# Performance work log

Hardware: AMD Instinct MI355X
Metric: run time of the kernel (lower is better)

Reference implementation:

```python
import jax, jax.numpy as jnp
import numpy as np
import math

B, S_IN, S_OUT, D_IN, D_OUT, G = 8, 1024, 1024, 96, 96, 8
LN_EPS = 1e-5


def setup_inputs() -> dict:
    key = jax.random.key(0)
    k_x, k_m, k_p, k_l = jax.random.split(key, 4)
    x = jax.random.normal(k_x, (B, S_IN, D_IN), dtype=jnp.float32)
    M = jax.random.uniform(k_m, (D_OUT, D_IN), minval=-0.5, maxval=0.5, dtype=jnp.float32)
    P = jax.random.uniform(k_p, (D_OUT, D_OUT, G), minval=-0.1, maxval=0.1, dtype=jnp.float32)
    Linker = jax.random.uniform(k_l, (S_IN, S_OUT), minval=-0.1, maxval=0.1, dtype=jnp.float32)
    gamma = jnp.ones((D_OUT,), dtype=jnp.float32)
    beta = jnp.zeros((D_OUT,), dtype=jnp.float32)
    return {"x": x, "M": M, "P": P, "Linker": Linker, "gamma": gamma, "beta": beta}


def _layer_norm(z, gamma, beta):
    mu = jnp.mean(z, axis=-1, keepdims=True)
    var = jnp.mean(jnp.square(z - mu), axis=-1, keepdims=True)
    return (z - mu) * jax.lax.rsqrt(var + LN_EPS) * gamma + beta


def reference(x, M, P, Linker, gamma, beta):
    # Z = x @ M^T, then LayerNorm over feature dim
    Z0 = jnp.einsum('bsj,ij->bsi', x, M)           # (B, S_in, D_out)
    Z = _layer_norm(Z0, gamma, beta)
    # periods[i,j,g] = i*(D_out*G) + j*G + g + 2
    periods = (jnp.arange(D_OUT * D_OUT * G, dtype=jnp.float32)
               .reshape(D_OUT, D_OUT, G) + 2.0)
    k = jnp.arange(S_IN, dtype=jnp.float32)
    # phi[s,i,j,g] = cos(2*pi*s / periods[i,j,g])
    phi = jnp.cos((2.0 * math.pi) * k[:, None, None, None] / periods[None])
    # fuse basis reduction: W[s,i,j] = sum_g P[i,j,g] * phi[s,i,j,g]
    W = jnp.einsum('sijg,ijg->sij', phi, P)        # (S_in, D_out, D_out)
    # T[b,s,i] = sum_j Z[b,s,j] * W[s,i,j]
    T = jnp.einsum('bsj,sij->bsi', Z, W)           # (B, S_in, D_out)
    # sequence transform via Linker
    U = jnp.einsum('bsi,st->bti', T, Linker)       # (B, S_out, D_out)
    # shared residual: x @ M^T (pre-LN) through the same Linker
    residual = jnp.einsum('bsi,st->bti', Z0, Linker)
    return U + residual
```

## Files before the change

### kernel.cpp

```cpp
#include <hip/hip_runtime.h>
#include <cstdint>
#include <cstddef>

#define NPAIR 9216
#define BSTRIDE 98304

typedef __attribute__((ext_vector_type(8))) short short8;
typedef __attribute__((ext_vector_type(4))) float f32x4;

__device__ __forceinline__ uint16_t f2bf(float x) {
    uint32_t u = __float_as_uint(x);
    return (uint16_t)((u + 0x7FFF + ((u >> 16) & 1)) >> 16);
}
__device__ __forceinline__ float bf2f(uint16_t b) {
    return __uint_as_float(((uint32_t)b) << 16);
}

union SmemK1 {
    float M[96][97];
    struct { float zb[16][100]; float ps[16][6][2]; float stats[16][2]; } ln;
    struct { float T[64][65]; } kl;
};

__global__ __launch_bounds__(96) void k1_mega(
    const float* __restrict__ x, const float* __restrict__ M,
    const float* __restrict__ P, const float* __restrict__ L,
    const float* __restrict__ gamma, const float* __restrict__ beta,
    float* __restrict__ Z0, float* __restrict__ Z,
    uint16_t* __restrict__ Lt, uint16_t* __restrict__ Wt)
{
    __shared__ SmemK1 sm;
    const int t  = threadIdx.x;
    const int bx = blockIdx.x;

    if (bx < 512) {
        const int R0 = bx * 16;
        for (int k = 0; k < 24; ++k) {
            int mm = t + 96 * k;
            int i = mm / 24, j0 = (mm % 24) * 4;
            float4 v = *(const float4*)(M + i * 96 + j0);
            sm.M[i][j0]   = v.x; sm.M[i][j0+1] = v.y;
            sm.M[i][j0+2] = v.z; sm.M[i][j0+3] = v.w;
        }
        __syncthreads();
        float mreg[96];
        #pragma unroll
        for (int j = 0; j < 96; ++j) mreg[j] = sm.M[t][j];
        __syncthreads();

        for (int r = 0; r < 16; ++r) {
            const float* xr = x + (size_t)(R0 + r) * 96;
            float a0 = 0.f, a1 = 0.f, a2 = 0.f, a3 = 0.f;
            #pragma unroll
            for (int j = 0; j < 96; j += 4) {
                a0 = fmaf(xr[j+0], mreg[j+0], a0);
                a1 = fmaf(xr[j+1], mreg[j+1], a1);
                a2 = fmaf(xr[j+2], mreg[j+2], a2);
                a3 = fmaf(xr[j+3], mreg[j+3], a3);
            }
            float z = (a0 + a1) + (a2 + a3);
            sm.ln.zb[r][t] = z;
            Z0[(size_t)(R0 + r) * 96 + t] = z;
        }
        __syncthreads();
        {
            const int row = t / 6, seg = t % 6;
            const float4* zp = (const float4*)&sm.ln.zb[row][seg * 16];
            float s1 = 0.f, s2 = 0.f;
            #pragma unroll
            for (int k = 0; k < 4; ++k) {
                float4 v = zp[k];
                s1 += v.x + v.y + v.z + v.w;
                s2 += v.x*v.x + v.y*v.y + v.z*v.z + v.w*v.w;
            }
            sm.ln.ps[row][seg][0] = s1;
            sm.ln.ps[row][seg][1] = s2;
        }
        __syncthreads();
        if (t < 16) {
            float s1 = 0.f, s2 = 0.f;
            #pragma unroll
            for (int k = 0; k < 6; ++k) {
                s1 += sm.ln.ps[t][k][0];
                s2 += sm.ln.ps[t][k][1];
            }
            float mu  = s1 * (1.f / 96.f);
            float var = s2 * (1.f / 96.f) - mu * mu;
            sm.ln.stats[t][0] = mu;
            sm.ln.stats[t][1] = rsqrtf(var + 1e-5f);
        }
        __syncthreads();
        {
            float gm = gamma[t], bt = beta[t];
            for (int r = 0; r < 16; ++r) {
                float mu = sm.ln.stats[r][0], rs = sm.ln.stats[r][1];
                Z[(size_t)(R0 + r) * 96 + t] =
                    (sm.ln.zb[r][t] - mu) * rs * gm + bt;
            }
        }
        return;
    }

    if (bx < 768) {
        const int bx2 = bx - 512;
        const int s0 = (bx2 & 15) * 64, t0 = (bx2 >> 4) * 64;
        if (t < 64) {
            for (int r = 0; r < 64; ++r)
                sm.kl.T[r][t] = L[(size_t)(s0 + r) * 1024 + t0 + t];
        }
        __syncthreads();
        if (t < 64) {
            uint16_t* orow = Lt + (size_t)(t0 + t) * 1024 + s0;
            #pragma unroll
            for (int c4 = 0; c4 < 16; ++c4) {
                uint32_t u01 = (uint32_t)f2bf(sm.kl.T[c4*4+0][t]) |
                               ((uint32_t)f2bf(sm.kl.T[c4*4+1][t]) << 16);
                uint32_t u23 = (uint32_t)f2bf(sm.kl.T[c4*4+2][t]) |
                               ((uint32_t)f2bf(sm.kl.T[c4*4+3][t]) << 16);
                uint2 o; o.x = u01; o.y = u23;
                *(uint2*)(orow + c4 * 4) = o;
            }
        }
        return;
    }

    {
        const int idx = bx - 768;
        const int pb  = idx % 96;
        const int sc  = idx / 96;
        const int p   = pb * 96 + t;
        const int i   = p % 96, j = p / 96;
        const int s0  = sc * 64;
        const int base = (i * 96 + j) * 8;

        float Pv[8], c[8], cp[8], tc1[8];
        {
            float4 a = *(const float4*)(P + base);
            float4 b = *(const float4*)(P + base + 4);
            Pv[0]=a.x; Pv[1]=a.y; Pv[2]=a.z; Pv[3]=a.w;
            Pv[4]=b.x; Pv[5]=b.y; Pv[6]=b.z; Pv[7]=b.w;
        }
        #pragma unroll
        for (int g = 0; g < 8; ++g) {
            float inv = 1.0f / (float)(base + g + 2);
            float c1  = cospif(2.0f * inv);
            tc1[g] = c1 + c1;
            c[g]  = cospif(2.0f * (float)s0 * inv);
            cp[g] = cospif(2.0f * (float)(s0 - 1) * inv);
        }
        uint16_t* op = Wt + (size_t)s0 * NPAIR + p;
        for (int ss = 0; ss < 64; ++ss) {
            float w = 0.f;
            #pragma unroll
            for (int g = 0; g < 8; ++g) w = fmaf(Pv[g], c[g], w);
            *op = f2bf(w);
            op += NPAIR;
            #pragma unroll
            for (int g = 0; g < 8; ++g) {
                float cn = fmaf(tc1[g], c[g], -cp[g]);
                cp[g] = c[g]; c[g] = cn;
            }
        }
    }
}

__global__ __launch_bounds__(96) void kt_apply(
    const float* __restrict__ Z, const float* __restrict__ Z0,
    const uint16_t* __restrict__ Wt, uint16_t* __restrict__ Vt)
{
    const int i = threadIdx.x;
    const int s = blockIdx.x;
    float acc[8] = {0.f,0.f,0.f,0.f,0.f,0.f,0.f,0.f};
    const uint16_t* wrow = Wt + (size_t)s * NPAIR + i;
    const float* zs = Z + (size_t)s * 96;
    #pragma unroll 8
    for (int j = 0; j < 96; ++j) {
        float w = bf2f(wrow[j * 96]);
        #pragma unroll
        for (int bb = 0; bb < 8; ++bb)
            acc[bb] = fmaf(zs[(size_t)bb * BSTRIDE + j], w, acc[bb]);
    }
    #pragma unroll
    for (int bb = 0; bb < 8; ++bb) {
        size_t o = (size_t)bb * BSTRIDE + (size_t)s * 96 + i;
        Vt[((size_t)bb * 96 + i) * 1024 + s] = f2bf(acc[bb] + Z0[o]);
    }
}

__global__ __launch_bounds__(128) void k3_mfma(
    const uint16_t* __restrict__ Lt, const uint16_t* __restrict__ Vt,
    float* __restrict__ out)
{
    const int lane = threadIdx.x & 63;
    const int wv   = threadIdx.x >> 6;
    const int m    = lane & 15;
    const int quad = lane >> 4;
    const int t0   = blockIdx.x * 32 + wv * 16;
    const int b    = blockIdx.y;

    const uint16_t* Lp = Lt + (size_t)(t0 + m) * 1024 + quad * 8;
    const uint16_t* Vp = Vt + ((size_t)b * 96 + m) * 1024 + quad * 8;

    f32x4 acc[6];
    #pragma unroll
    for (int ii = 0; ii < 6; ++ii) acc[ii] = (f32x4){0.f, 0.f, 0.f, 0.f};

    short8 a = *(const short8*)Lp;
    short8 bv[6];
    #pragma unroll
    for (int ii = 0; ii < 6; ++ii)
        bv[ii] = *(const short8*)(Vp + (size_t)ii * 16 * 1024);

    for (int kc = 0; kc < 31; ++kc) {
        short8 an = *(const short8*)(Lp + (kc + 1) * 32);
        short8 bn[6];
        #pragma unroll
        for (int ii = 0; ii < 6; ++ii)
            bn[ii] = *(const short8*)(Vp + (size_t)ii * 16 * 1024 + (kc + 1) * 32);
        #pragma unroll
        for (int ii = 0; ii < 6; ++ii)
            acc[ii] = __builtin_amdgcn_mfma_f32_16x16x32_bf16(a, bv[ii], acc[ii], 0, 0, 0);
        a = an;
        #pragma unroll
        for (int ii = 0; ii < 6; ++ii) bv[ii] = bn[ii];
    }
    #pragma unroll
    for (int ii = 0; ii < 6; ++ii)
        acc[ii] = __builtin_amdgcn_mfma_f32_16x16x32_bf16(a, bv[ii], acc[ii], 0, 0, 0);

    float* po = out + (size_t)b * BSTRIDE;
    #pragma unroll
    for (int ii = 0; ii < 6; ++ii)
        #pragma unroll
        for (int r = 0; r < 4; ++r)
            po[(size_t)(t0 + quad * 4 + r) * 96 + ii * 16 + m] = acc[ii][r];
}

extern "C" void kernel_launch(void* const* d_in, const int* in_sizes, int n_in,
                              void* d_out, int out_size, void* d_ws, size_t ws_size,
                              hipStream_t stream)
{
    const float* x     = (const float*)d_in[0];
    const float* M     = (const float*)d_in[1];
    const float* P     = (const float*)d_in[2];
    const float* Lnk   = (const float*)d_in[3];
    const float* gamma = (const float*)d_in[4];
    const float* beta  = (const float*)d_in[5];
    float* out = (float*)d_out;

    uint8_t* ws = (uint8_t*)d_ws;
    uint16_t* Wt = (uint16_t*)ws;
    float*    Z0 = (float*)(ws + 18874368);
    float*    Z  = (float*)(ws + 22020096);
    uint16_t* Lt = (uint16_t*)(ws + 25165824);
    uint16_t* Vt = (uint16_t*)(ws + 27262976);

    k1_mega <<<2304, 96, 0, stream>>>(x, M, P, Lnk, gamma, beta, Z0, Z, Lt, Wt);
    kt_apply<<<1024, 96, 0, stream>>>(Z, Z0, Wt, Vt);
    k3_mfma <<<dim3(32, 8), 128, 0, stream>>>(Lt, Vt, out);
}
```

Measured before the change: 125.2 us.

## Rebalance work split across all three kernels with split-K MFMA and wider blocks

k1_mega now runs 256-thread blocks: each LayerNorm block handles two 32-row groups and loads M straight into registers without going through shared memory. The Linker transpose uses 16 blocks that loop over the whole sequence, and the W-basis generation is packed at 256 threads per block. kt_apply splits the batch into two halves to double the block count. k3_mfma splits K across four waves and reduces the partial results through shared memory, giving more blocks. The aim is better occupancy and latency hiding, at the cost of an extra LDS reduction and syncs, and a serialized transpose that now runs on only 16 blocks.

```diff
diff --git a/kernel.cpp b/kernel.cpp
--- a/kernel.cpp
+++ b/kernel.cpp
@@ -17,12 +17,11 @@
 }
 
 union SmemK1 {
-    float M[96][97];
-    struct { float zb[16][100]; float ps[16][6][2]; float stats[16][2]; } ln;
-    struct { float T[64][65]; } kl;
+    struct { float zb[2][32][100]; float ps[2][32][3][2]; float stats[2][32][2]; } ln;
+    struct { float T[64][17]; } kl;
 };
 
-__global__ __launch_bounds__(96) void k1_mega(
+__global__ __launch_bounds__(256) void k1_mega(
     const float* __restrict__ x, const float* __restrict__ M,
     const float* __restrict__ P, const float* __restrict__ L,
     const float* __restrict__ gamma, const float* __restrict__ beta,
@@ -33,104 +32,98 @@
     const int t  = threadIdx.x;
     const int bx = blockIdx.x;
 
-    if (bx < 512) {
-        const int R0 = bx * 16;
-        for (int k = 0; k < 24; ++k) {
-            int mm = t + 96 * k;
-            int i = mm / 24, j0 = (mm % 24) * 4;
-            float4 v = *(const float4*)(M + i * 96 + j0);
-            sm.M[i][j0]   = v.x; sm.M[i][j0+1] = v.y;
-            sm.M[i][j0+2] = v.z; sm.M[i][j0+3] = v.w;
+    if (bx < 128) {
+        const int g = t >> 7, lt = t & 127;
+        const int R0 = bx * 64 + g * 32;
+        if (lt < 96) {
+            float mreg[96];
+            #pragma unroll
+            for (int k4 = 0; k4 < 24; ++k4) {
+                float4 v = *(const float4*)(M + lt * 96 + k4 * 4);
+                mreg[k4*4+0]=v.x; mreg[k4*4+1]=v.y;
+                mreg[k4*4+2]=v.z; mreg[k4*4+3]=v.w;
+            }
+            for (int r = 0; r < 32; ++r) {
+                const float* xr = x + (size_t)(R0 + r) * 96;
+                float a0 = 0.f, a1 = 0.f, a2 = 0.f, a3 = 0.f;
+                #pragma unroll
+                for (int j = 0; j < 96; j += 4) {
+                    a0 = fmaf(xr[j+0], mreg[j+0], a0);
+                    a1 = fmaf(xr[j+1], mreg[j+1], a1);
+                    a2 = fmaf(xr[j+2], mreg[j+2], a2);
+                    a3 = fmaf(xr[j+3], mreg[j+3], a3);
+                }
+                float z = (a0 + a1) + (a2 + a3);
+                sm.ln.zb[g][r][lt] = z;
+                Z0[(size_t)(R0 + r) * 96 + lt] = z;
+            }
         }
         __syncthreads();
-        float mreg[96];
-        #pragma unroll
-        for (int j = 0; j < 96; ++j) mreg[j] = sm.M[t][j];
+        if (lt < 96) {
+            int row = lt / 3, seg = lt % 3;
+            const float4* zp = (const float4*)&sm.ln.zb[g][row][seg * 32];
+            float s1 = 0.f, s2 = 0.f;
+            #pragma unroll
+            for (int k = 0; k < 8; ++k) {
+                float4 v = zp[k];
+                s1 += (v.x + v.y) + (v.z + v.w);
+                s2 += (v.x*v.x + v.y*v.y) + (v.z*v.z + v.w*v.w);
+            }
+            sm.ln.ps[g][row][seg][0] = s1;
+            sm.ln.ps[g][row][seg][1] = s2;
+        }
         __syncthreads();
-
-        for (int r = 0; r < 16; ++r) {
-            const float* xr = x + (size_t)(R0 + r) * 96;
-            float a0 = 0.f, a1 = 0.f, a2 = 0.f, a3 = 0.f;
-            #pragma unroll
-            for (int j = 0; j < 96; j += 4) {
-                a0 = fmaf(xr[j+0], mreg[j+0], a0);
-                a1 = fmaf(xr[j+1], mreg[j+1], a1);
-                a2 = fmaf(xr[j+2], mreg[j+2], a2);
-                a3 = fmaf(xr[j+3], mreg[j+3], a3);
-            }
-            float z = (a0 + a1) + (a2 + a3);
-            sm.ln.zb[r][t] = z;
-            Z0[(size_t)(R0 + r) * 96 + t] = z;
-        }
-        __syncthreads();
-        {
-            const int row = t / 6, seg = t % 6;
-            const float4* zp = (const float4*)&sm.ln.zb[row][seg * 16];
-            float s1 = 0.f, s2 = 0.f;
-            #pragma unroll
-            for (int k = 0; k < 4; ++k) {
-                float4 v = zp[k];
-                s1 += v.x + v.y + v.z + v.w;
-                s2 += v.x*v.x + v.y*v.y + v.z*v.z + v.w*v.w;
-            }
-            sm.ln.ps[row][seg][0] = s1;
-            sm.ln.ps[row][seg][1] = s2;
-        }
-        __syncthreads();
-        if (t < 16) {
-            float s1 = 0.f, s2 = 0.f;
-            #pragma unroll
-            for (int k = 0; k < 6; ++k) {
-                s1 += sm.ln.ps[t][k][0];
-                s2 += sm.ln.ps[t][k][1];
-            }
+        if (lt < 32) {
+            float s1 = sm.ln.ps[g][lt][0][0] + sm.ln.ps[g][lt][1][0] + sm.ln.ps[g][lt][2][0];
+            float s2 = sm.ln.ps[g][lt][0][1] + sm.ln.ps[g][lt][1][1] + sm.ln.ps[g][lt][2][1];
             float mu  = s1 * (1.f / 96.f);
             float var = s2 * (1.f / 96.f) - mu * mu;
-            sm.ln.stats[t][0] = mu;
-            sm.ln.stats[t][1] = rsqrtf(var + 1e-5f);
+            sm.ln.stats[g][lt][0] = mu;
+            sm.ln.stats[g][lt][1] = rsqrtf(var + 1e-5f);
         }
         __syncthreads();
-        {
-            float gm = gamma[t], bt = beta[t];
-            for (int r = 0; r < 16; ++r) {
-                float mu = sm.ln.stats[r][0], rs = sm.ln.stats[r][1];
-                Z[(size_t)(R0 + r) * 96 + t] =
-                    (sm.ln.zb[r][t] - mu) * rs * gm + bt;
+        if (lt < 96) {
+            float gm = gamma[lt], bt = beta[lt];
+            for (int r = 0; r < 32; ++r) {
+                float mu = sm.ln.stats[g][r][0], rs = sm.ln.stats[g][r][1];
+                Z[(size_t)(R0 + r) * 96 + lt] = (sm.ln.zb[g][r][lt] - mu) * rs * gm + bt;
             }
         }
         return;
     }
 
-    if (bx < 768) {
-        const int bx2 = bx - 512;
-        const int s0 = (bx2 & 15) * 64, t0 = (bx2 >> 4) * 64;
-        if (t < 64) {
-            for (int r = 0; r < 64; ++r)
-                sm.kl.T[r][t] = L[(size_t)(s0 + r) * 1024 + t0 + t];
-        }
-        __syncthreads();
-        if (t < 64) {
-            uint16_t* orow = Lt + (size_t)(t0 + t) * 1024 + s0;
-            #pragma unroll
-            for (int c4 = 0; c4 < 16; ++c4) {
-                uint32_t u01 = (uint32_t)f2bf(sm.kl.T[c4*4+0][t]) |
-                               ((uint32_t)f2bf(sm.kl.T[c4*4+1][t]) << 16);
-                uint32_t u23 = (uint32_t)f2bf(sm.kl.T[c4*4+2][t]) |
-                               ((uint32_t)f2bf(sm.kl.T[c4*4+3][t]) << 16);
-                uint2 o; o.x = u01; o.y = u23;
-                *(uint2*)(orow + c4 * 4) = o;
+    if (bx < 144) {
+        for (int cgi = 0; cgi < 4; ++cgi) {
+            const int t0 = (bx - 128) * 64 + cgi * 16;
+            const int tx = t & 15, ty = t >> 4;
+            for (int s0 = 0; s0 < 1024; s0 += 64) {
+                #pragma unroll
+                for (int k = 0; k < 4; ++k) {
+                    int sr = ty + k * 16;
+                    sm.kl.T[sr][tx] = L[(size_t)(s0 + sr) * 1024 + t0 + tx];
+                }
+                __syncthreads();
+                {
+                    int trow = t >> 4, sc = (t & 15) * 4;
+                    uint32_t u01 = (uint32_t)f2bf(sm.kl.T[sc+0][trow]) |
+                                   ((uint32_t)f2bf(sm.kl.T[sc+1][trow]) << 16);
+                    uint32_t u23 = (uint32_t)f2bf(sm.kl.T[sc+2][trow]) |
+                                   ((uint32_t)f2bf(sm.kl.T[sc+3][trow]) << 16);
+                    uint2 o; o.x = u01; o.y = u23;
+                    *(uint2*)(Lt + (size_t)(t0 + trow) * 1024 + s0 + sc) = o;
+                }
+                __syncthreads();
             }
         }
         return;
     }
 
     {
-        const int idx = bx - 768;
-        const int pb  = idx % 96;
-        const int sc  = idx / 96;
-        const int p   = pb * 96 + t;
-        const int i   = p % 96, j = p / 96;
-        const int s0  = sc * 64;
+        const int u  = (bx - 144) * 256 + t;
+        const int p  = u % 9216;
+        const int sc = u / 9216;
+        const int i  = p % 96, j = p / 96;
+        const int s0 = sc * 64;
         const int base = (i * 96 + j) * 8;
 
         float Pv[8], c[8], cp[8], tc1[8];
@@ -168,38 +161,40 @@
     const float* __restrict__ Z, const float* __restrict__ Z0,
     const uint16_t* __restrict__ Wt, uint16_t* __restrict__ Vt)
 {
-    const int i = threadIdx.x;
-    const int s = blockIdx.x;
-    float acc[8] = {0.f,0.f,0.f,0.f,0.f,0.f,0.f,0.f};
+    const int i  = threadIdx.x;
+    const int s  = blockIdx.x >> 1;
+    const int b0 = (blockIdx.x & 1) * 4;
+    float acc[4] = {0.f, 0.f, 0.f, 0.f};
     const uint16_t* wrow = Wt + (size_t)s * NPAIR + i;
-    const float* zs = Z + (size_t)s * 96;
+    const float* zs = Z + (size_t)b0 * BSTRIDE + (size_t)s * 96;
     #pragma unroll 8
     for (int j = 0; j < 96; ++j) {
         float w = bf2f(wrow[j * 96]);
         #pragma unroll
-        for (int bb = 0; bb < 8; ++bb)
+        for (int bb = 0; bb < 4; ++bb)
             acc[bb] = fmaf(zs[(size_t)bb * BSTRIDE + j], w, acc[bb]);
     }
     #pragma unroll
-    for (int bb = 0; bb < 8; ++bb) {
-        size_t o = (size_t)bb * BSTRIDE + (size_t)s * 96 + i;
-        Vt[((size_t)bb * 96 + i) * 1024 + s] = f2bf(acc[bb] + Z0[o]);
-    }
-}
-
-__global__ __launch_bounds__(128) void k3_mfma(
+    for (int bb = 0; bb < 4; ++bb) {
+        size_t o = (size_t)(b0 + bb) * BSTRIDE + (size_t)s * 96 + i;
+        Vt[((size_t)(b0 + bb) * 96 + i) * 1024 + s] = f2bf(acc[bb] + Z0[o]);
+    }
+}
+
+__global__ __launch_bounds__(256) void k3_mfma(
     const uint16_t* __restrict__ Lt, const uint16_t* __restrict__ Vt,
     float* __restrict__ out)
 {
+    __shared__ float red[4][64][25];
     const int lane = threadIdx.x & 63;
     const int wv   = threadIdx.x >> 6;
     const int m    = lane & 15;
     const int quad = lane >> 4;
-    const int t0   = blockIdx.x * 32 + wv * 16;
+    const int t0   = blockIdx.x * 16;
     const int b    = blockIdx.y;
 
-    const uint16_t* Lp = Lt + (size_t)(t0 + m) * 1024 + quad * 8;
-    const uint16_t* Vp = Vt + ((size_t)b * 96 + m) * 1024 + quad * 8;
+    const uint16_t* Lp = Lt + (size_t)(t0 + m) * 1024 + wv * 256 + quad * 8;
+    const uint16_t* Vp = Vt + ((size_t)b * 96 + m) * 1024 + wv * 256 + quad * 8;
 
     f32x4 acc[6];
     #pragma unroll
@@ -211,7 +206,7 @@
     for (int ii = 0; ii < 6; ++ii)
         bv[ii] = *(const short8*)(Vp + (size_t)ii * 16 * 1024);
 
-    for (int kc = 0; kc < 31; ++kc) {
+    for (int kc = 0; kc < 7; ++kc) {
         short8 an = *(const short8*)(Lp + (kc + 1) * 32);
         short8 bn[6];
         #pragma unroll
@@ -228,12 +223,24 @@
     for (int ii = 0; ii < 6; ++ii)
         acc[ii] = __builtin_amdgcn_mfma_f32_16x16x32_bf16(a, bv[ii], acc[ii], 0, 0, 0);
 
-    float* po = out + (size_t)b * BSTRIDE;
     #pragma unroll
     for (int ii = 0; ii < 6; ++ii)
         #pragma unroll
         for (int r = 0; r < 4; ++r)
-            po[(size_t)(t0 + quad * 4 + r) * 96 + ii * 16 + m] = acc[ii][r];
+            red[wv][lane][ii * 4 + r] = acc[ii][r];
+    __syncthreads();
+    {
+        const int l2 = threadIdx.x & 63;
+        const int ks = (threadIdx.x >> 6) * 6;
+        const int m2 = l2 & 15, q2 = l2 >> 4;
+        #pragma unroll
+        for (int k = ks; k < ks + 6; ++k) {
+            float sv = red[0][l2][k] + red[1][l2][k]
+                     + red[2][l2][k] + red[3][l2][k];
+            int ii = k >> 2, r = k & 3;
+            out[(size_t)b * BSTRIDE + (size_t)(t0 + q2 * 4 + r) * 96 + ii * 16 + m2] = sv;
+        }
+    }
 }
 
 extern "C" void kernel_launch(void* const* d_in, const int* in_sizes, int n_in,
@@ -255,7 +262,7 @@
     uint16_t* Lt = (uint16_t*)(ws + 25165824);
     uint16_t* Vt = (uint16_t*)(ws + 27262976);
 
-    k1_mega <<<2304, 96, 0, stream>>>(x, M, P, Lnk, gamma, beta, Z0, Z, Lt, Wt);
-    kt_apply<<<1024, 96, 0, stream>>>(Z, Z0, Wt, Vt);
-    k3_mfma <<<dim3(32, 8), 128, 0, stream>>>(Lt, Vt, out);
-}
+    k1_mega <<<720,  256, 0, stream>>>(x, M, P, Lnk, gamma, beta, Z0, Z, Lt, Wt);
+    kt_apply<<<2048, 96,  0, stream>>>(Z, Z0, Wt, Vt);
+    k3_mfma <<<dim3(64, 8), 256, 0, stream>>>(Lt, Vt, out);
+}
```

Measured after the change: 131.5 us. 5.0% more time.

## Halve W-generation chunk and restructure kt_apply to two positions per block

Applied to the files above, without the earlier changes.

The W-basis generation blocks in k1_mega now cover 32 sequence positions instead of 64, and the grid grows so there are more blocks to spread the recurrence work. kt_apply now runs 192 threads per block, each handling two adjacent sequence positions and four batches. The two bf16 outputs are packed into one 32-bit store to Vt instead of two scattered 16-bit stores. The aim is more parallelism and better-coalesced writes, at the cost of more cospif setup per generated element and different reuse of Z loads.

```diff
diff --git a/kernel.cpp b/kernel.cpp
--- a/kernel.cpp
+++ b/kernel.cpp
@@ -130,7 +130,7 @@
         const int sc  = idx / 96;
         const int p   = pb * 96 + t;
         const int i   = p % 96, j = p / 96;
-        const int s0  = sc * 64;
+        const int s0  = sc * 32;
         const int base = (i * 96 + j) * 8;
 
         float Pv[8], c[8], cp[8], tc1[8];
@@ -149,7 +149,8 @@
             cp[g] = cospif(2.0f * (float)(s0 - 1) * inv);
         }
         uint16_t* op = Wt + (size_t)s0 * NPAIR + p;
-        for (int ss = 0; ss < 64; ++ss) {
+        #pragma unroll 4
+        for (int ss = 0; ss < 32; ++ss) {
             float w = 0.f;
             #pragma unroll
             for (int g = 0; g < 8; ++g) w = fmaf(Pv[g], c[g], w);
@@ -164,26 +165,36 @@
     }
 }
 
-__global__ __launch_bounds__(96) void kt_apply(
+__global__ __launch_bounds__(192) void kt_apply(
     const float* __restrict__ Z, const float* __restrict__ Z0,
     const uint16_t* __restrict__ Wt, uint16_t* __restrict__ Vt)
 {
-    const int i = threadIdx.x;
-    const int s = blockIdx.x;
-    float acc[8] = {0.f,0.f,0.f,0.f,0.f,0.f,0.f,0.f};
-    const uint16_t* wrow = Wt + (size_t)s * NPAIR + i;
-    const float* zs = Z + (size_t)s * 96;
-    #pragma unroll 8
+    const int i  = threadIdx.x % 96;
+    const int b0 = (threadIdx.x / 96) * 4;
+    const int s0 = blockIdx.x * 2;
+    float acc0[4] = {0.f, 0.f, 0.f, 0.f};
+    float acc1[4] = {0.f, 0.f, 0.f, 0.f};
+    const uint16_t* w0 = Wt + (size_t)s0 * NPAIR + i;
+    const uint16_t* w1 = w0 + NPAIR;
+    const float* z0p = Z + (size_t)b0 * BSTRIDE + (size_t)s0 * 96;
+    const float* z1p = z0p + 96;
+    #pragma unroll 4
     for (int j = 0; j < 96; ++j) {
-        float w = bf2f(wrow[j * 96]);
-        #pragma unroll
-        for (int bb = 0; bb < 8; ++bb)
-            acc[bb] = fmaf(zs[(size_t)bb * BSTRIDE + j], w, acc[bb]);
-    }
-    #pragma unroll
-    for (int bb = 0; bb < 8; ++bb) {
-        size_t o = (size_t)bb * BSTRIDE + (size_t)s * 96 + i;
-        Vt[((size_t)bb * 96 + i) * 1024 + s] = f2bf(acc[bb] + Z0[o]);
+        float wa = bf2f(w0[j * 96]);
+        float wb = bf2f(w1[j * 96]);
+        #pragma unroll
+        for (int bb = 0; bb < 4; ++bb) {
+            acc0[bb] = fmaf(z0p[(size_t)bb * BSTRIDE + j], wa, acc0[bb]);
+            acc1[bb] = fmaf(z1p[(size_t)bb * BSTRIDE + j], wb, acc1[bb]);
+        }
+    }
+    #pragma unroll
+    for (int bb = 0; bb < 4; ++bb) {
+        const int b = b0 + bb;
+        size_t o0 = (size_t)b * BSTRIDE + (size_t)s0 * 96 + i;
+        uint32_t lo = f2bf(acc0[bb] + Z0[o0]);
+        uint32_t hi = f2bf(acc1[bb] + Z0[o0 + 96]);
+        *(uint32_t*)(Vt + ((size_t)b * 96 + i) * 1024 + s0) = lo | (hi << 16);
     }
 }
 
@@ -255,7 +266,7 @@
     uint16_t* Lt = (uint16_t*)(ws + 25165824);
     uint16_t* Vt = (uint16_t*)(ws + 27262976);
 
-    k1_mega <<<2304, 96, 0, stream>>>(x, M, P, Lnk, gamma, beta, Z0, Z, Lt, Wt);
-    kt_apply<<<1024, 96, 0, stream>>>(Z, Z0, Wt, Vt);
+    k1_mega <<<3840, 96, 0, stream>>>(x, M, P, Lnk, gamma, beta, Z0, Z, Lt, Wt);
+    kt_apply<<<512, 192, 0, stream>>>(Z, Z0, Wt, Vt);
     k3_mfma <<<dim3(32, 8), 128, 0, stream>>>(Lt, Vt, out);
 }
```

Measured after the change: 129.4 us. 3.3% more time.
